# Kernel tuning notes

Hardware: AMD Instinct MI355X
Metric: run time of the kernel (lower is better)

The kernel has to match this reference:

```python
import jax, jax.numpy as jnp
import numpy as np

N = 100000       # nodes
E = 3200000      # edges (avg degree 32)
IN_F = 256
OUT_F = 128
LRELU_ALPHA = 0.2
EPS = 1e-16


def setup_inputs() -> dict:
    key = jax.random.key(0)
    k1, k2, k3, k4 = jax.random.split(key, 4)
    x = jax.random.normal(k1, (N, IN_F), dtype=jnp.float32)
    edge_index = jax.random.randint(k2, (2, E), 0, N, dtype=jnp.int32)
    # xavier_uniform with gain=calculate_gain('relu')=sqrt(2)
    gain = float(np.sqrt(2.0))
    bw = gain * float(np.sqrt(6.0 / (IN_F + OUT_F)))
    weight = jax.random.uniform(k3, (IN_F, OUT_F), dtype=jnp.float32, minval=-bw, maxval=bw)
    ba = gain * float(np.sqrt(6.0 / (1 + 2 * OUT_F)))
    a = jax.random.uniform(k4, (1, 2 * OUT_F), dtype=jnp.float32, minval=-ba, maxval=ba)
    return {"x": x, "edge_index": edge_index, "weight": weight, "a": a}


def reference(x, edge_index, weight, a):
    src = edge_index[0]
    dst = edge_index[1]
    h = x @ weight                                  # [N, OUT_F]
    # e_edge = a @ cat(h[src], h[dst]) == (h @ a_l)[src] + (h @ a_r)[dst]
    a_l = a[0, :OUT_F]
    a_r = a[0, OUT_F:]
    s_l = h @ a_l                                   # [N]
    s_r = h @ a_r                                   # [N]
    e = s_l[src] + s_r[dst]                         # [E]
    e = jnp.where(e >= 0, e, LRELU_ALPHA * e)       # LeakyReLU
    # segment softmax over src groups
    e_max = jax.ops.segment_max(e, src, num_segments=N)   # [N]
    e_exp = jnp.exp(e - e_max[src])                        # [E]
    denom = jax.ops.segment_sum(e_exp, src, num_segments=N)[src] + EPS
    alpha_e = e_exp / denom                                # [E]
    # out[src] += alpha_e * h[dst]  (sparse A_alpha @ h)
    out = jax.ops.segment_sum(alpha_e[:, None] * h[dst], src, num_segments=N)
    return out
```

## Files before the change

kernel.cpp:

```cpp
#include <hip/hip_runtime.h>

#define GN 100000
#define GE 3200000
#define CAP 128
#define NB 391
#define CHUNK 4096

typedef __attribute__((ext_vector_type(8))) short bf16x8;
typedef __attribute__((ext_vector_type(4))) float f32x4;

__device__ __forceinline__ unsigned short f2bf(float f) {
    unsigned u = __float_as_uint(f);
    u += 0x7fffu + ((u >> 16) & 1u);
    return (unsigned short)(u >> 16);
}

__global__ __launch_bounds__(256) void wprep_kernel(const float* __restrict__ w,
                                                    unsigned short* __restrict__ wT) {
    int flat4 = blockIdx.x * 256 + threadIdx.x;
    if (flat4 >= 256 * 128 / 4) return;
    int k  = flat4 >> 5;
    int n4 = (flat4 & 31) * 4;
    float4 v = ((const float4*)w)[flat4];
    wT[(size_t)(n4 + 0) * 256 + k] = f2bf(v.x);
    wT[(size_t)(n4 + 1) * 256 + k] = f2bf(v.y);
    wT[(size_t)(n4 + 2) * 256 + k] = f2bf(v.z);
    wT[(size_t)(n4 + 3) * 256 + k] = f2bf(v.w);
}

__global__ __launch_bounds__(256) void gemm_kernel(const float* __restrict__ x,
                                                   const unsigned short* __restrict__ wT,
                                                   const float* __restrict__ a,
                                                   unsigned short* __restrict__ hq,
                                                   float* __restrict__ s_l,
                                                   float* __restrict__ s_r) {
    __shared__ unsigned short As[128][40];
    const int tid  = threadIdx.x;
    const int lane = tid & 63, wid = tid >> 6;
    const int l16  = lane & 15, quad = lane >> 4;
    const int wm   = (wid >> 1) * 64, wn = (wid & 1) * 64;
    const int bm   = blockIdx.x * 128;

    f32x4 acc[4][4] = {};

    const int arow = tid >> 1, ahalf = tid & 1;
    int gr = bm + arow; if (gr >= GN) gr = GN - 1;
    const float* xrow = x + (size_t)gr * 256 + ahalf * 16;

    for (int k0 = 0; k0 < 256; k0 += 32) {
        float4 f0 = *(const float4*)(xrow + k0);
        float4 f1 = *(const float4*)(xrow + k0 + 4);
        float4 f2 = *(const float4*)(xrow + k0 + 8);
        float4 f3 = *(const float4*)(xrow + k0 + 12);
        bf16x8 s0, s1;
        s0[0] = f2bf(f0.x); s0[1] = f2bf(f0.y); s0[2] = f2bf(f0.z); s0[3] = f2bf(f0.w);
        s0[4] = f2bf(f1.x); s0[5] = f2bf(f1.y); s0[6] = f2bf(f1.z); s0[7] = f2bf(f1.w);
        s1[0] = f2bf(f2.x); s1[1] = f2bf(f2.y); s1[2] = f2bf(f2.z); s1[3] = f2bf(f2.w);
        s1[4] = f2bf(f3.x); s1[5] = f2bf(f3.y); s1[6] = f2bf(f3.z); s1[7] = f2bf(f3.w);
        __syncthreads();
        *(bf16x8*)&As[arow][ahalf * 16]     = s0;
        *(bf16x8*)&As[arow][ahalf * 16 + 8] = s1;
        __syncthreads();
        bf16x8 af[4], bfr[4];
#pragma unroll
        for (int t = 0; t < 4; ++t) {
            af[t]  = *(const bf16x8*)&As[wm + t * 16 + l16][quad * 8];
            bfr[t] = *(const bf16x8*)(wT + (size_t)(wn + t * 16 + l16) * 256 + k0 + quad * 8);
        }
#pragma unroll
        for (int ti = 0; ti < 4; ++ti)
#pragma unroll
            for (int tj = 0; tj < 4; ++tj)
                acc[ti][tj] = __builtin_amdgcn_mfma_f32_16x16x32_bf16(af[ti], bfr[tj], acc[ti][tj], 0, 0, 0);
    }

    float alv[4], arv[4];
#pragma unroll
    for (int tj = 0; tj < 4; ++tj) {
        alv[tj] = a[wn + tj * 16 + l16];
        arv[tj] = a[128 + wn + tj * 16 + l16];
    }
#pragma unroll
    for (int ti = 0; ti < 4; ++ti) {
        float slp[4], srp[4];
#pragma unroll
        for (int r = 0; r < 4; ++r) {
            int row = bm + wm + ti * 16 + quad * 4 + r;
            float v0 = acc[ti][0][r], v1 = acc[ti][1][r], v2 = acc[ti][2][r], v3 = acc[ti][3][r];
            if (row < GN) {
                unsigned short* hp = hq + (size_t)row * 128 + wn + l16;
                hp[0]  = f2bf(v0);
                hp[16] = f2bf(v1);
                hp[32] = f2bf(v2);
                hp[48] = f2bf(v3);
            }
            slp[r] = v0 * alv[0] + v1 * alv[1] + v2 * alv[2] + v3 * alv[3];
            srp[r] = v0 * arv[0] + v1 * arv[1] + v2 * arv[2] + v3 * arv[3];
        }
#pragma unroll
        for (int off = 1; off < 16; off <<= 1)
#pragma unroll
            for (int r = 0; r < 4; ++r) {
                slp[r] += __shfl_xor(slp[r], off, 64);
                srp[r] += __shfl_xor(srp[r], off, 64);
            }
        if (l16 == 0) {
#pragma unroll
            for (int r = 0; r < 4; ++r) {
                int row = bm + wm + ti * 16 + quad * 4 + r;
                if (row < GN) {
                    atomicAdd(&s_l[row], slp[r]);
                    atomicAdd(&s_r[row], srp[r]);
                }
            }
        }
    }
}

__global__ __launch_bounds__(256) void bhist_kernel(const int* __restrict__ src,
                                                    int* __restrict__ bcnt) {
    __shared__ int bh[NB];
    const int tid = threadIdx.x;
    for (int j = tid; j < NB; j += 256) bh[j] = 0;
    __syncthreads();
    const int base = blockIdx.x * CHUNK;
    const int cnt = min(CHUNK, GE - base);
    for (int i = tid; i < cnt; i += 256) atomicAdd(&bh[src[base + i] >> 8], 1);
    __syncthreads();
    for (int j = tid; j < NB; j += 256)
        if (bh[j]) atomicAdd(&bcnt[j], bh[j]);
}

__global__ __launch_bounds__(64) void bscan_kernel(const int* __restrict__ bcnt,
                                                   int* __restrict__ bbase,
                                                   int* __restrict__ bcursor) {
    __shared__ int arr[NB];
    const int tid = threadIdx.x;
    for (int j = tid; j < NB; j += 64) arr[j] = bcnt[j];
    __syncthreads();
    int carry = 0;
    for (int b0 = 0; b0 < NB; b0 += 64) {
        int idx = b0 + tid;
        int v = (idx < NB) ? arr[idx] : 0;
        int x = v;
#pragma unroll
        for (int off = 1; off < 64; off <<= 1) {
            int y = __shfl_up(x, off, 64);
            if (tid >= off) x += y;
        }
        if (idx < NB) { bbase[idx] = carry + x - v; bcursor[idx] = carry + x - v; }
        carry += __shfl(x, 63, 64);
    }
    if (tid == 0) bbase[NB] = carry;
}

__global__ __launch_bounds__(256) void bin_kernel(const int* __restrict__ ei,
                                                  int* __restrict__ bcursor,
                                                  unsigned* __restrict__ binned) {
    __shared__ int h_cnt[NB];
    __shared__ int h_base[NB + 1];
    __shared__ int h_gpos[NB];
    __shared__ int h_cur[NB];
    __shared__ unsigned sbuf[CHUNK];
    __shared__ unsigned short sbkt[CHUNK];
    const int tid = threadIdx.x;
    const int base = blockIdx.x * CHUNK;
    const int cnt = min(CHUNK, GE - base);

    int srcv[CHUNK / 256], dstv[CHUNK / 256];
#pragma unroll
    for (int i = 0; i < CHUNK / 256; ++i) {
        int idx = tid + i * 256;
        if (idx < cnt) { srcv[i] = ei[base + idx]; dstv[i] = ei[GE + base + idx]; }
        else srcv[i] = -1;
    }
    for (int j = tid; j < NB; j += 256) h_cnt[j] = 0;
    __syncthreads();
#pragma unroll
    for (int i = 0; i < CHUNK / 256; ++i)
        if (srcv[i] >= 0) atomicAdd(&h_cnt[srcv[i] >> 8], 1);
    __syncthreads();
    if (tid < 64) {
        int carry = 0;
        for (int b0 = 0; b0 < NB; b0 += 64) {
            int idx = b0 + tid;
            int v = (idx < NB) ? h_cnt[idx] : 0;
            int x = v;
#pragma unroll
            for (int off = 1; off < 64; off <<= 1) {
                int y = __shfl_up(x, off, 64);
                if (tid >= off) x += y;
            }
            if (idx < NB) h_base[idx] = carry + x - v;
            carry += __shfl(x, 63, 64);
        }
        if (tid == 0) h_base[NB] = carry;
    }
    __syncthreads();
    for (int j = tid; j < NB; j += 256) {
        h_cur[j] = h_base[j];
        int c = h_cnt[j];
        if (c) h_gpos[j] = atomicAdd(&bcursor[j], c);
    }
    __syncthreads();
#pragma unroll
    for (int i = 0; i < CHUNK / 256; ++i)
        if (srcv[i] >= 0) {
            int b = srcv[i] >> 8;
            int p = atomicAdd(&h_cur[b], 1);
            sbuf[p] = ((unsigned)(srcv[i] & 255) << 17) | (unsigned)dstv[i];
            sbkt[p] = (unsigned short)b;
        }
    __syncthreads();
    for (int p = tid; p < cnt; p += 256) {
        int b = sbkt[p];
        binned[h_gpos[b] + (p - h_base[b])] = sbuf[p];
    }
}

__global__ __launch_bounds__(256) void fine_kernel(const unsigned* __restrict__ binned,
                                                   const int* __restrict__ bbase,
                                                   int* __restrict__ rowptr,
                                                   int* __restrict__ adj) {
    __shared__ int n_cnt[256];
    __shared__ int n_base[257];
    __shared__ int n_cur[256];
    const int b = blockIdx.x;
    const int tid = threadIdx.x;
    const int node0 = b * 256;
    const int nn = min(256, GN - node0);
    const int beg = bbase[b], end = bbase[b + 1];
    n_cnt[tid] = 0;
    __syncthreads();
    for (int p = beg + tid; p < end; p += 256)
        atomicAdd(&n_cnt[binned[p] >> 17], 1);
    __syncthreads();
    if (tid < 64) {
        int carry = 0;
        for (int b0 = 0; b0 < 256; b0 += 64) {
            int idx = b0 + tid;
            int v = n_cnt[idx];
            int x = v;
#pragma unroll
            for (int off = 1; off < 64; off <<= 1) {
                int y = __shfl_up(x, off, 64);
                if (tid >= off) x += y;
            }
            n_base[idx] = carry + x - v;
            carry += __shfl(x, 63, 64);
        }
        if (tid == 0) n_base[256] = carry;
    }
    __syncthreads();
    if (tid < nn) rowptr[node0 + tid] = beg + n_base[tid];
    if (b == NB - 1 && tid == 0) rowptr[GN] = end;
    n_cur[tid] = n_base[tid];
    __syncthreads();
    for (int p = beg + tid; p < end; p += 256) {
        unsigned e = binned[p];
        int s = e >> 17, d = (int)(e & 0x1FFFFu);
        int pos = atomicAdd(&n_cur[s], 1);
        adj[beg + pos] = d;
    }
}

__global__ __launch_bounds__(256) void aggregate_kernel(const uint4* __restrict__ h4,
                                                        const float* __restrict__ s_l,
                                                        const float* __restrict__ s_r,
                                                        const int* __restrict__ rowptr,
                                                        const int* __restrict__ adj,
                                                        float* __restrict__ out) {
    __shared__ int   s_dst[4][CAP];
    __shared__ float s_w[4][CAP];
    const int wid = threadIdx.x >> 6, lane = threadIdx.x & 63;
    const int node = blockIdx.x * 4 + wid;
    const int beg = rowptr[node], end = rowptr[node + 1];
    const int deg = end - beg;
    const float sl = s_l[node];

    float m = -1e30f;
    for (int j = lane; j < deg; j += 64) {
        int dst = adj[beg + j];
        float e = sl + s_r[dst];
        e = (e >= 0.f) ? e : 0.2f * e;
        if (j < CAP) { s_dst[wid][j] = dst; s_w[wid][j] = e; }
        m = fmaxf(m, e);
    }
#pragma unroll
    for (int off = 1; off < 64; off <<= 1)
        m = fmaxf(m, __shfl_xor(m, off, 64));
    __syncthreads();

    const int n2 = deg < CAP ? deg : CAP;
    float d = 0.f;
    for (int j = lane; j < n2; j += 64) {
        float w = __expf(s_w[wid][j] - m);
        s_w[wid][j] = w;
        d += w;
    }
    for (int j = CAP + lane; j < deg; j += 64) {
        int dst = adj[beg + j];
        float e = sl + s_r[dst];
        e = (e >= 0.f) ? e : 0.2f * e;
        d += __expf(e - m);
    }
#pragma unroll
    for (int off = 1; off < 64; off <<= 1)
        d += __shfl_xor(d, off, 64);
    const float inv = 1.f / (d + 1e-16f);
    __syncthreads();

    const int fl = lane & 15, grp = lane >> 4;
    f32x4 accA = {0.f, 0.f, 0.f, 0.f}, accB = {0.f, 0.f, 0.f, 0.f};
    int j = 0;
#pragma unroll 2
    for (; j < n2; j += 8) {
        int j0 = j + grp, j1 = j + grp + 4;
        bool a0 = j0 < n2, a1 = j1 < n2;
        int   d0 = s_dst[wid][a0 ? j0 : 0];
        int   d1 = s_dst[wid][a1 ? j1 : 0];
        float w0 = a0 ? s_w[wid][j0] : 0.f;
        float w1 = a1 ? s_w[wid][j1] : 0.f;
        uint4 v0 = h4[(size_t)d0 * 16 + fl];
        uint4 v1 = h4[(size_t)d1 * 16 + fl];
        accA.x += w0 * __uint_as_float(v0.x << 16);
        accA.y += w0 * __uint_as_float(v0.x & 0xffff0000u);
        accA.z += w0 * __uint_as_float(v0.y << 16);
        accA.w += w0 * __uint_as_float(v0.y & 0xffff0000u);
        accB.x += w0 * __uint_as_float(v0.z << 16);
        accB.y += w0 * __uint_as_float(v0.z & 0xffff0000u);
        accB.z += w0 * __uint_as_float(v0.w << 16);
        accB.w += w0 * __uint_as_float(v0.w & 0xffff0000u);
        accA.x += w1 * __uint_as_float(v1.x << 16);
        accA.y += w1 * __uint_as_float(v1.x & 0xffff0000u);
        accA.z += w1 * __uint_as_float(v1.y << 16);
        accA.w += w1 * __uint_as_float(v1.y & 0xffff0000u);
        accB.x += w1 * __uint_as_float(v1.z << 16);
        accB.y += w1 * __uint_as_float(v1.z & 0xffff0000u);
        accB.z += w1 * __uint_as_float(v1.w << 16);
        accB.w += w1 * __uint_as_float(v1.w & 0xffff0000u);
    }
    for (; j < deg; j += 4) {
        int jj = j + grp;
        bool act = jj < deg;
        int dst = act ? adj[beg + jj] : 0;
        float e = sl + s_r[dst];
        e = (e >= 0.f) ? e : 0.2f * e;
        float w = act ? __expf(e - m) : 0.f;
        uint4 v = h4[(size_t)dst * 16 + fl];
        accA.x += w * __uint_as_float(v.x << 16);
        accA.y += w * __uint_as_float(v.x & 0xffff0000u);
        accA.z += w * __uint_as_float(v.y << 16);
        accA.w += w * __uint_as_float(v.y & 0xffff0000u);
        accB.x += w * __uint_as_float(v.z << 16);
        accB.y += w * __uint_as_float(v.z & 0xffff0000u);
        accB.z += w * __uint_as_float(v.w << 16);
        accB.w += w * __uint_as_float(v.w & 0xffff0000u);
    }

#pragma unroll
    for (int off = 16; off < 64; off <<= 1) {
        accA.x += __shfl_xor(accA.x, off, 64);
        accA.y += __shfl_xor(accA.y, off, 64);
        accA.z += __shfl_xor(accA.z, off, 64);
        accA.w += __shfl_xor(accA.w, off, 64);
        accB.x += __shfl_xor(accB.x, off, 64);
        accB.y += __shfl_xor(accB.y, off, 64);
        accB.z += __shfl_xor(accB.z, off, 64);
        accB.w += __shfl_xor(accB.w, off, 64);
    }
    if (lane < 16) {
        float* orow = out + (size_t)node * 128 + fl * 8;
        accA.x *= inv; accA.y *= inv; accA.z *= inv; accA.w *= inv;
        accB.x *= inv; accB.y *= inv; accB.z *= inv; accB.w *= inv;
        *(f32x4*)orow       = accA;
        *(f32x4*)(orow + 4) = accB;
    }
}

extern "C" void kernel_launch(void* const* d_in, const int* in_sizes, int n_in,
                              void* d_out, int out_size, void* d_ws, size_t ws_size,
                              hipStream_t stream) {
    const float* x  = (const float*)d_in[0];
    const int*   ei = (const int*)d_in[1];
    const float* w  = (const float*)d_in[2];
    const float* a  = (const float*)d_in[3];
    float* out = (float*)d_out;

    unsigned short* hq = (unsigned short*)d_ws;
    float* s_l     = (float*)(hq + (size_t)GN * 128);
    float* s_r     = s_l + GN;
    int*   bcnt    = (int*)(s_r + GN);
    int*   bbase   = bcnt + NB;
    int*   bcursor = bbase + NB + 1;
    int*   rowptr  = bcursor + NB;
    unsigned* binned = (unsigned*)(rowptr + GN + 1);
    int*   adj     = (int*)(binned + GE);
    unsigned short* wT = (unsigned short*)(adj + GE);

    hipMemsetAsync(s_l, 0, (size_t)(2 * GN + NB) * sizeof(float), stream);

    wprep_kernel<<<32, 256, 0, stream>>>(w, wT);
    gemm_kernel<<<(GN + 127) / 128, 256, 0, stream>>>(x, wT, a, hq, s_l, s_r);
    bhist_kernel<<<(GE + CHUNK - 1) / CHUNK, 256, 0, stream>>>(ei, bcnt);
    bscan_kernel<<<1, 64, 0, stream>>>(bcnt, bbase, bcursor);
    bin_kernel<<<(GE + CHUNK - 1) / CHUNK, 256, 0, stream>>>(ei, bcursor, binned);
    fine_kernel<<<NB, 256, 0, stream>>>(binned, bbase, rowptr, adj);
    aggregate_kernel<<<GN / 4, 256, 0, stream>>>((const uint4*)hq, s_l, s_r, rowptr, adj, out);
}
```

Measured before the change: 406.8 us.

## Double-buffer GEMM LDS tiles with register prefetch; widen fine_kernel to 1024 threads

The GEMM main loop now uses two LDS buffers for the x tile and prefetches the next K-slice of x and wT into registers while MFMAs run on the current slice. This halves the barriers per iteration and hides global load latency. Separately, fine_kernel runs 1024 threads per block instead of 256, so each of the 391 bucket blocks gets more parallelism for its counting and scatter loops. The trade-offs are higher register pressure in the GEMM and more LDS atomic contention in fine_kernel.

Result: no change. 399.1 us (-1.9%).

```diff
diff --git a/kernel.cpp b/kernel.cpp
--- a/kernel.cpp
+++ b/kernel.cpp
@@ -34,7 +34,7 @@
                                                    unsigned short* __restrict__ hq,
                                                    float* __restrict__ s_l,
                                                    float* __restrict__ s_r) {
-    __shared__ unsigned short As[128][40];
+    __shared__ unsigned short As[2][128][40];
     const int tid  = threadIdx.x;
     const int lane = tid & 63, wid = tid >> 6;
     const int l16  = lane & 15, quad = lane >> 4;
@@ -47,31 +47,60 @@
     int gr = bm + arow; if (gr >= GN) gr = GN - 1;
     const float* xrow = x + (size_t)gr * 256 + ahalf * 16;
 
-    for (int k0 = 0; k0 < 256; k0 += 32) {
-        float4 f0 = *(const float4*)(xrow + k0);
-        float4 f1 = *(const float4*)(xrow + k0 + 4);
-        float4 f2 = *(const float4*)(xrow + k0 + 8);
-        float4 f3 = *(const float4*)(xrow + k0 + 12);
+    {
+        float4 f0 = *(const float4*)(xrow + 0);
+        float4 f1 = *(const float4*)(xrow + 4);
+        float4 f2 = *(const float4*)(xrow + 8);
+        float4 f3 = *(const float4*)(xrow + 12);
         bf16x8 s0, s1;
         s0[0] = f2bf(f0.x); s0[1] = f2bf(f0.y); s0[2] = f2bf(f0.z); s0[3] = f2bf(f0.w);
         s0[4] = f2bf(f1.x); s0[5] = f2bf(f1.y); s0[6] = f2bf(f1.z); s0[7] = f2bf(f1.w);
         s1[0] = f2bf(f2.x); s1[1] = f2bf(f2.y); s1[2] = f2bf(f2.z); s1[3] = f2bf(f2.w);
         s1[4] = f2bf(f3.x); s1[5] = f2bf(f3.y); s1[6] = f2bf(f3.z); s1[7] = f2bf(f3.w);
-        __syncthreads();
-        *(bf16x8*)&As[arow][ahalf * 16]     = s0;
-        *(bf16x8*)&As[arow][ahalf * 16 + 8] = s1;
-        __syncthreads();
-        bf16x8 af[4], bfr[4];
-#pragma unroll
-        for (int t = 0; t < 4; ++t) {
-            af[t]  = *(const bf16x8*)&As[wm + t * 16 + l16][quad * 8];
-            bfr[t] = *(const bf16x8*)(wT + (size_t)(wn + t * 16 + l16) * 256 + k0 + quad * 8);
-        }
+        *(bf16x8*)&As[0][arow][ahalf * 16]     = s0;
+        *(bf16x8*)&As[0][arow][ahalf * 16 + 8] = s1;
+    }
+    bf16x8 bcur[4];
+#pragma unroll
+    for (int t = 0; t < 4; ++t)
+        bcur[t] = *(const bf16x8*)(wT + (size_t)(wn + t * 16 + l16) * 256 + quad * 8);
+    __syncthreads();
+
+#pragma unroll
+    for (int ks = 0; ks < 8; ++ks) {
+        const int cb = ks & 1;
+        bf16x8 bnxt[4];
+        bf16x8 s0, s1;
+        if (ks < 7) {
+            const int k1 = (ks + 1) * 32;
+#pragma unroll
+            for (int t = 0; t < 4; ++t)
+                bnxt[t] = *(const bf16x8*)(wT + (size_t)(wn + t * 16 + l16) * 256 + k1 + quad * 8);
+            float4 f0 = *(const float4*)(xrow + k1);
+            float4 f1 = *(const float4*)(xrow + k1 + 4);
+            float4 f2 = *(const float4*)(xrow + k1 + 8);
+            float4 f3 = *(const float4*)(xrow + k1 + 12);
+            s0[0] = f2bf(f0.x); s0[1] = f2bf(f0.y); s0[2] = f2bf(f0.z); s0[3] = f2bf(f0.w);
+            s0[4] = f2bf(f1.x); s0[5] = f2bf(f1.y); s0[6] = f2bf(f1.z); s0[7] = f2bf(f1.w);
+            s1[0] = f2bf(f2.x); s1[1] = f2bf(f2.y); s1[2] = f2bf(f2.z); s1[3] = f2bf(f2.w);
+            s1[4] = f2bf(f3.x); s1[5] = f2bf(f3.y); s1[6] = f2bf(f3.z); s1[7] = f2bf(f3.w);
+        }
+        bf16x8 af[4];
+#pragma unroll
+        for (int t = 0; t < 4; ++t)
+            af[t] = *(const bf16x8*)&As[cb][wm + t * 16 + l16][quad * 8];
 #pragma unroll
         for (int ti = 0; ti < 4; ++ti)
 #pragma unroll
             for (int tj = 0; tj < 4; ++tj)
-                acc[ti][tj] = __builtin_amdgcn_mfma_f32_16x16x32_bf16(af[ti], bfr[tj], acc[ti][tj], 0, 0, 0);
+                acc[ti][tj] = __builtin_amdgcn_mfma_f32_16x16x32_bf16(af[ti], bcur[tj], acc[ti][tj], 0, 0, 0);
+        if (ks < 7) {
+            *(bf16x8*)&As[cb ^ 1][arow][ahalf * 16]     = s0;
+            *(bf16x8*)&As[cb ^ 1][arow][ahalf * 16 + 8] = s1;
+            __syncthreads();
+#pragma unroll
+            for (int t = 0; t < 4; ++t) bcur[t] = bnxt[t];
+        }
     }
 
     float alv[4], arv[4];
@@ -218,10 +247,10 @@
     }
 }
 
-__global__ __launch_bounds__(256) void fine_kernel(const unsigned* __restrict__ binned,
-                                                   const int* __restrict__ bbase,
-                                                   int* __restrict__ rowptr,
-                                                   int* __restrict__ adj) {
+__global__ __launch_bounds__(1024) void fine_kernel(const unsigned* __restrict__ binned,
+                                                    const int* __restrict__ bbase,
+                                                    int* __restrict__ rowptr,
+                                                    int* __restrict__ adj) {
     __shared__ int n_cnt[256];
     __shared__ int n_base[257];
     __shared__ int n_cur[256];
@@ -230,9 +259,9 @@
     const int node0 = b * 256;
     const int nn = min(256, GN - node0);
     const int beg = bbase[b], end = bbase[b + 1];
-    n_cnt[tid] = 0;
-    __syncthreads();
-    for (int p = beg + tid; p < end; p += 256)
+    if (tid < 256) n_cnt[tid] = 0;
+    __syncthreads();
+    for (int p = beg + tid; p < end; p += 1024)
         atomicAdd(&n_cnt[binned[p] >> 17], 1);
     __syncthreads();
     if (tid < 64) {
@@ -254,9 +283,9 @@
     __syncthreads();
     if (tid < nn) rowptr[node0 + tid] = beg + n_base[tid];
     if (b == NB - 1 && tid == 0) rowptr[GN] = end;
-    n_cur[tid] = n_base[tid];
-    __syncthreads();
-    for (int p = beg + tid; p < end; p += 256) {
+    if (tid < 256) n_cur[tid] = n_base[tid];
+    __syncthreads();
+    for (int p = beg + tid; p < end; p += 1024) {
         unsigned e = binned[p];
         int s = e >> 17, d = (int)(e & 0x1FFFFu);
         int pos = atomicAdd(&n_cur[s], 1);
@@ -405,6 +434,6 @@
     bhist_kernel<<<(GE + CHUNK - 1) / CHUNK, 256, 0, stream>>>(ei, bcnt);
     bscan_kernel<<<1, 64, 0, stream>>>(bcnt, bbase, bcursor);
     bin_kernel<<<(GE + CHUNK - 1) / CHUNK, 256, 0, stream>>>(ei, bcursor, binned);
-    fine_kernel<<<NB, 256, 0, stream>>>(binned, bbase, rowptr, adj);
+    fine_kernel<<<NB, 1024, 0, stream>>>(binned, bbase, rowptr, adj);
     aggregate_kernel<<<GN / 4, 256, 0, stream>>>((const uint4*)hq, s_l, s_r, rowptr, adj, out);
 }
```
